# Optimization experiments

Hardware: AMD Instinct MI355X
Metric: run time of the kernel (lower is better)

## Reference

```python
import jax, jax.numpy as jnp
import numpy as np

DILATIONS = (1, 2, 4, 8, 16, 32, 64, 128, 256)
R = 128          # residual/skip channels
K = 3            # kernel size
B, CIN, T = 8, 1, 16384
COUT = 1
L = len(DILATIONS)


def causal_conv(x, w, b, dilation):
    # x: [B, Cin, T], w: [Cout, Cin, K] -> [B, Cout, T], left-padded (causal)
    k = w.shape[-1]
    pad = dilation * (k - 1)
    y = jax.lax.conv_general_dilated(
        x, w, window_strides=(1,), padding=[(pad, 0)],
        rhs_dilation=(dilation,), dimension_numbers=("NCH", "OIH", "NCH"))
    return y + b[None, :, None]


def setup_inputs() -> dict:
    key = jax.random.key(0)
    ks = jax.random.split(key, 11)
    s = 0.1  # weight scale to keep gated activations in a healthy range
    return {
        "x": jax.random.normal(ks[0], (B, CIN, T), jnp.float32),
        "input_w": s * jax.random.normal(ks[1], (R, CIN, 1), jnp.float32),
        "input_b": s * jax.random.normal(ks[2], (R,), jnp.float32),
        "conv_w": s * jax.random.normal(ks[3], (L, 2 * R, R, K), jnp.float32),
        "conv_b": s * jax.random.normal(ks[4], (L, 2 * R), jnp.float32),
        "out_w": s * jax.random.normal(ks[5], (L, R, R, 1), jnp.float32),
        "out_b": s * jax.random.normal(ks[6], (L, R), jnp.float32),
        "output1_w": s * jax.random.normal(ks[7], (R, R * L, 1), jnp.float32),
        "output1_b": s * jax.random.normal(ks[8], (R,), jnp.float32),
        "output2_w": s * jax.random.normal(ks[9], (COUT, R, 1), jnp.float32),
        "output2_b": s * jax.random.normal(ks[10], (COUT,), jnp.float32),
    }


def reference(x, input_w, input_b, conv_w, conv_b, out_w, out_b,
              output1_w, output1_b, output2_w, output2_b):
    # input layer: 1x1 conv + tanh (use_output_transform=False)
    h = jnp.tanh(causal_conv(x, input_w, input_b, 1))

    skips = []
    for i, d in enumerate(DILATIONS):
        pre = causal_conv(h, conv_w[i], conv_b[i], d)      # [B, 2R, T]
        t, g = jnp.split(pre, 2, axis=1)
        z = jnp.tanh(t) * jax.nn.sigmoid(g)                # gated activation
        skips.append(z)                                     # skip = activation out
        res = causal_conv(z, out_w[i], out_b[i], 1)         # 1x1 output transform
        h = h + res                                         # residual connection

    sk = jnp.concatenate(skips, axis=1)                     # [B, R*L, T]
    y = jnp.tanh(causal_conv(sk, output1_w, output1_b, 1))
    out = causal_conv(y, output2_w, output2_b, 1)           # linear
    return out
```

## Files before the change

### kernel.cpp

```cpp
#include <hip/hip_runtime.h>
#include <cstdint>
#include <cstddef>

#define T_LEN 16384
#define BATCH 8
#define NLAYER 9

typedef _Float16 f16;
typedef __attribute__((ext_vector_type(8))) _Float16 f16x8;
typedef __attribute__((ext_vector_type(4))) float f32x4;
#define MFMA_F16 __builtin_amdgcn_mfma_f32_16x16x32_f16

__device__ __forceinline__ float fast_sigmoid(float x) {
    return 1.0f / (1.0f + __expf(-x));
}
__device__ __forceinline__ float fast_tanh(float x) {
    return 1.0f - 2.0f / (__expf(2.0f * x) + 1.0f);
}

__device__ __forceinline__ void stage16(const f16* g, f16* l) {
    __builtin_amdgcn_global_load_lds(
        (const __attribute__((address_space(1))) unsigned int*)g,
        (__attribute__((address_space(3))) unsigned int*)l, 16, 0, 0);
}

__global__ __launch_bounds__(256) void prep_weights(
    const float* __restrict__ cw, const float* __restrict__ ow,
    const float* __restrict__ o1w, f16* __restrict__ wA, f16* __restrict__ wB)
{
    int n = blockIdx.x * 256 + threadIdx.x;
    const int NA = NLAYER * 12 * 256 * 32;
    const int NB = NLAYER * 4 * 256 * 32;
    if (n < NA) {
        int kp = n & 31; int q = n >> 5;
        int c = q & 255; q >>= 8;
        int ch = q % 12; int l = q / 12;
        int i = kp >> 3, j = kp & 7;
        int il = i ^ ((c >> 1) & 3);
        int kpl = il * 8 + j;
        int tap = ch >> 2;
        int r = (ch & 3) * 32 + kpl;
        wA[n] = (f16)cw[((size_t)(l * 256 + c) * 128 + r) * 3 + tap];
    } else if (n < NA + NB) {
        int m = n - NA;
        int kp = m & 31; int q = m >> 5;
        int c = q & 255; q >>= 8;
        int ch = q & 3; int l = q >> 2;
        int k = ch * 32 + kp;
        float v = (c < 128) ? ow[(size_t)(l * 128 + c) * 128 + k]
                            : o1w[(size_t)(c - 128) * 1152 + l * 128 + k];
        wB[m] = (f16)v;
    }
}

__global__ __launch_bounds__(256) void input_init(
    const float* __restrict__ x, const float* __restrict__ iw,
    const float* __restrict__ ib,
    f16* __restrict__ h, f16* __restrict__ acc1)
{
    int n = blockIdx.x * 256 + threadIdx.x;
    int r = n & 127; int bt = n >> 7;
    h[n] = (f16)fast_tanh(iw[r] * x[bt] + ib[r]);
    acc1[n] = (f16)0.0f;
}

__global__ __launch_bounds__(256, 4) void layer_kernel(
    const f16* __restrict__ h_in, f16* __restrict__ h_out,
    f16* __restrict__ acc1,
    const f16* __restrict__ wA,
    const f16* __restrict__ wB,
    const float* __restrict__ cb,
    const float* __restrict__ ob,
    int d)
{
    __shared__ __align__(16) char smem_raw[32768];
    f16* const Bsm = (f16*)smem_raw;
    f16* const zs  = (f16*)smem_raw;

    const int tid  = threadIdx.x;
    const int lane = tid & 63;
    const int w4   = tid >> 6;
    const int mg   = w4 & 1;
    const int ng   = w4 >> 1;
    const int col  = lane & 15;
    const int quad = lane >> 4;
    const int b    = blockIdx.y;
    const int bx   = blockIdx.x;
    const int xt   = ((bx & 7) << 5) | (bx >> 3);
    const int t0   = xt * 64;

    const f16* hb = h_in + (size_t)b * T_LEN * 128;

    const int bswz = (quad ^ ((col >> 1) & 3)) * 8;

    f32x4 acc[2][8];
#pragma unroll
    for (int mt = 0; mt < 2; ++mt)
#pragma unroll
        for (int nt = 0; nt < 8; ++nt) acc[mt][nt] = (f32x4)0.0f;

    {
        const f16* src = wA + w4 * 2048 + lane * 8;
        f16* dst = Bsm + w4 * 2048;
#pragma unroll
        for (int i = 0; i < 4; ++i) stage16(src + i * 512, dst + i * 512);
    }

#pragma unroll
    for (int tap = 0; tap < 3; ++tap) {
        const int off = (2 - tap) * d;
        f16x8 a[2][4];
#pragma unroll
        for (int c = 0; c < 4; ++c) {
            const int ch = tap * 4 + c;
            __builtin_amdgcn_sched_barrier(0);
            asm volatile("s_waitcnt vmcnt(0)" ::: "memory");
            __builtin_amdgcn_s_barrier();
            __builtin_amdgcn_sched_barrier(0);
            if (ch < 11) {
                const f16* src = wA + (ch + 1) * 8192 + w4 * 2048 + lane * 8;
                f16* dst = Bsm + ((ch + 1) & 1) * 8192 + w4 * 2048;
#pragma unroll
                for (int i = 0; i < 4; ++i) stage16(src + i * 512, dst + i * 512);
            }
            if (c == 0) {
#pragma unroll
                for (int mt = 0; mt < 2; ++mt) {
                    int t = t0 + mg * 32 + mt * 16 + col - off;
                    if (t >= 0) {
                        const f16* hp = &hb[(size_t)t * 128 + quad * 8];
#pragma unroll
                        for (int cc = 0; cc < 4; ++cc)
                            a[mt][cc] = *(const f16x8*)&hp[cc * 32];
                    } else {
#pragma unroll
                        for (int cc = 0; cc < 4; ++cc)
                            a[mt][cc] = (f16x8)(f16)0.0f;
                    }
                }
            }
            const f16* bsc = Bsm + (ch & 1) * 8192;
#pragma unroll
            for (int nt = 0; nt < 8; ++nt) {
                int nb = (nt < 4) ? (ng * 64 + nt * 16)
                                  : (128 + ng * 64 + (nt - 4) * 16);
                f16x8 bf = *(const f16x8*)&bsc[(nb + col) * 32 + bswz];
                acc[0][nt] = MFMA_F16(a[0][c], bf, acc[0][nt], 0, 0, 0);
                acc[1][nt] = MFMA_F16(a[1][c], bf, acc[1][nt], 0, 0, 0);
            }
        }
    }
    __syncthreads();

#pragma unroll
    for (int nt = 0; nt < 4; ++nt) {
        int j = ng * 64 + nt * 16 + col;
        float cf = cb[j];
        float cg = cb[j + 128];
#pragma unroll
        for (int mt = 0; mt < 2; ++mt)
#pragma unroll
            for (int reg = 0; reg < 4; ++reg) {
                float f = acc[mt][nt][reg]     + cf;
                float g = acc[mt][nt + 4][reg] + cg;
                zs[(mg * 32 + mt * 16 + quad * 4 + reg) * 136 + j] =
                    (f16)(fast_tanh(f) * fast_sigmoid(g));
            }
    }
    __syncthreads();

#pragma unroll
    for (int mt = 0; mt < 2; ++mt)
#pragma unroll
        for (int nt = 0; nt < 8; ++nt) acc[mt][nt] = (f32x4)0.0f;

#pragma unroll
    for (int ch = 0; ch < 4; ++ch) {
        f16x8 a[2];
#pragma unroll
        for (int mt = 0; mt < 2; ++mt)
            a[mt] = *(const f16x8*)&zs[(mg * 32 + mt * 16 + col) * 136 + ch * 32 + quad * 8];
        const f16* wc = wB + ch * 8192;
#pragma unroll
        for (int nt = 0; nt < 8; ++nt) {
            int nb = (nt < 4) ? (ng * 64 + nt * 16)
                              : (128 + ng * 64 + (nt - 4) * 16);
            f16x8 bf = *(const f16x8*)&wc[(nb + col) * 32 + quad * 8];
            acc[0][nt] = MFMA_F16(a[0], bf, acc[0][nt], 0, 0, 0);
            acc[1][nt] = MFMA_F16(a[1], bf, acc[1][nt], 0, 0, 0);
        }
    }
    __syncthreads();

#pragma unroll
    for (int nt = 0; nt < 4; ++nt) {
        int n = ng * 64 + nt * 16 + col;
        float o = ob[n];
#pragma unroll
        for (int mt = 0; mt < 2; ++mt)
#pragma unroll
            for (int reg = 0; reg < 4; ++reg)
                zs[(mg * 32 + mt * 16 + quad * 4 + reg) * 136 + n] =
                    (f16)(acc[mt][nt][reg] + o);
    }
    __syncthreads();
    const int orow = tid >> 2, oseg = tid & 3;
    const size_t gb = (size_t)b * T_LEN * 128 + (size_t)(t0 + orow) * 128 + oseg * 32;
#pragma unroll
    for (int i = 0; i < 4; ++i) {
        f16x8 rv = *(const f16x8*)&zs[orow * 136 + oseg * 32 + i * 8];
        f16x8 hv = *(const f16x8*)&h_in[gb + i * 8];
        *(f16x8*)&h_out[gb + i * 8] = hv + rv;
    }
    __syncthreads();

#pragma unroll
    for (int nt = 0; nt < 4; ++nt) {
        int n = ng * 64 + nt * 16 + col;
#pragma unroll
        for (int mt = 0; mt < 2; ++mt)
#pragma unroll
            for (int reg = 0; reg < 4; ++reg)
                zs[(mg * 32 + mt * 16 + quad * 4 + reg) * 136 + n] =
                    (f16)acc[mt][nt + 4][reg];
    }
    __syncthreads();
#pragma unroll
    for (int i = 0; i < 4; ++i) {
        f16x8 sv2 = *(const f16x8*)&zs[orow * 136 + oseg * 32 + i * 8];
        f16x8 av  = *(const f16x8*)&acc1[gb + i * 8];
        *(f16x8*)&acc1[gb + i * 8] = av + sv2;
    }
}

__global__ __launch_bounds__(256) void final_kernel(
    const f16* __restrict__ acc1, const float* __restrict__ b1,
    const float* __restrict__ w2, const float* __restrict__ b2,
    float* __restrict__ out)
{
    int lane = threadIdx.x & 63;
    int w = threadIdx.x >> 6;
    int bt = blockIdx.x * 4 + w;
    float v0 = (float)acc1[(size_t)bt * 128 + lane];
    float v1 = (float)acc1[(size_t)bt * 128 + lane + 64];
    float s = w2[lane] * fast_tanh(v0 + b1[lane]) +
              w2[lane + 64] * fast_tanh(v1 + b1[lane + 64]);
#pragma unroll
    for (int k = 1; k < 64; k <<= 1) s += __shfl_xor(s, k, 64);
    if (lane == 0) out[bt] = s + b2[0];
}

extern "C" void kernel_launch(void* const* d_in, const int* in_sizes, int n_in,
                              void* d_out, int out_size, void* d_ws, size_t ws_size,
                              hipStream_t stream)
{
    const float* x   = (const float*)d_in[0];
    const float* iw  = (const float*)d_in[1];
    const float* ib  = (const float*)d_in[2];
    const float* cw  = (const float*)d_in[3];
    const float* cb  = (const float*)d_in[4];
    const float* ow  = (const float*)d_in[5];
    const float* ob  = (const float*)d_in[6];
    const float* o1w = (const float*)d_in[7];
    const float* o1b = (const float*)d_in[8];
    const float* o2w = (const float*)d_in[9];
    const float* o2b = (const float*)d_in[10];
    float* out = (float*)d_out;

    const size_t HTR = (size_t)BATCH * T_LEN * 128;
    f16* hA   = (f16*)d_ws;
    f16* hB   = hA + HTR;
    f16* acc1 = hB + HTR;
    f16* wAp  = acc1 + HTR;
    f16* wBp  = wAp + (size_t)NLAYER * 12 * 256 * 32;

    prep_weights<<<4608, 256, 0, stream>>>(cw, ow, o1w, wAp, wBp);
    input_init<<<65536, 256, 0, stream>>>(x, iw, ib, hA, acc1);

    const int DIL[NLAYER] = {1, 2, 4, 8, 16, 32, 64, 128, 256};
    f16* hin = hA; f16* hout = hB;
    for (int l = 0; l < NLAYER; ++l) {
        layer_kernel<<<dim3(T_LEN / 64, BATCH), 256, 0, stream>>>(
            hin, hout, acc1,
            wAp + (size_t)l * 12 * 256 * 32, wBp + (size_t)l * 4 * 256 * 32,
            cb + l * 256, ob + l * 128, DIL[l]);
        f16* tmp = hin; hin = hout; hout = tmp;
    }
    final_kernel<<<BATCH * T_LEN / 4, 256, 0, stream>>>(acc1, o1b, o2w, o2b, out);
}
```

Before: 812.7 us.

## Deepen weight staging pipeline, prefetch taps, merge epilogue LDS passes

```diff
diff --git a/kernel.cpp b/kernel.cpp
--- a/kernel.cpp
+++ b/kernel.cpp
@@ -11,17 +11,14 @@
 typedef __attribute__((ext_vector_type(4))) float f32x4;
 #define MFMA_F16 __builtin_amdgcn_mfma_f32_16x16x32_f16
 
-__device__ __forceinline__ float fast_sigmoid(float x) {
-    return 1.0f / (1.0f + __expf(-x));
-}
-__device__ __forceinline__ float fast_tanh(float x) {
-    return 1.0f - 2.0f / (__expf(2.0f * x) + 1.0f);
-}
-
 __device__ __forceinline__ void stage16(const f16* g, f16* l) {
     __builtin_amdgcn_global_load_lds(
         (const __attribute__((address_space(1))) unsigned int*)g,
         (__attribute__((address_space(3))) unsigned int*)l, 16, 0, 0);
+}
+
+__device__ __forceinline__ float fast_tanh(float x) {
+    return 1.0f - 2.0f / (__expf(2.0f * x) + 1.0f);
 }
 
 __global__ __launch_bounds__(256) void prep_weights(
@@ -73,9 +70,10 @@
     const float* __restrict__ ob,
     int d)
 {
-    __shared__ __align__(16) char smem_raw[32768];
+    __shared__ __align__(16) char smem_raw[34816];
     f16* const Bsm = (f16*)smem_raw;
-    f16* const zs  = (f16*)smem_raw;
+    f16* const zsR = (f16*)smem_raw;
+    f16* const zsS = (f16*)smem_raw + 8704;
 
     const int tid  = threadIdx.x;
     const int lane = tid & 63;
@@ -90,7 +88,6 @@
     const int t0   = xt * 64;
 
     const f16* hb = h_in + (size_t)b * T_LEN * 128;
-
     const int bswz = (quad ^ ((col >> 1) & 3)) * 8;
 
     f32x4 acc[2][8];
@@ -99,56 +96,64 @@
 #pragma unroll
         for (int nt = 0; nt < 8; ++nt) acc[mt][nt] = (f32x4)0.0f;
 
+    f16x8 a[2][4];
+    auto loadA = [&](int tap) {
+        const int off = (2 - tap) * d;
+#pragma unroll
+        for (int mt = 0; mt < 2; ++mt) {
+            int t = t0 + mg * 32 + mt * 16 + col - off;
+            int tc = t < 0 ? 0 : t;
+            const f16* hp = &hb[(size_t)tc * 128 + quad * 8];
+#pragma unroll
+            for (int cc = 0; cc < 4; ++cc) {
+                f16x8 v = *(const f16x8*)&hp[cc * 32];
+                a[mt][cc] = (t >= 0) ? v : (f16x8)(f16)0.0f;
+            }
+        }
+    };
+
     {
-        const f16* src = wA + w4 * 2048 + lane * 8;
-        f16* dst = Bsm + w4 * 2048;
-#pragma unroll
-        for (int i = 0; i < 4; ++i) stage16(src + i * 512, dst + i * 512);
-    }
-
-#pragma unroll
-    for (int tap = 0; tap < 3; ++tap) {
-        const int off = (2 - tap) * d;
-        f16x8 a[2][4];
-#pragma unroll
-        for (int c = 0; c < 4; ++c) {
-            const int ch = tap * 4 + c;
-            __builtin_amdgcn_sched_barrier(0);
+        const f16* s0 = wA + w4 * 1024 + lane * 8;
+        f16* d0 = Bsm + w4 * 1024;
+        stage16(s0, d0); stage16(s0 + 512, d0 + 512);
+        const f16* s1 = wA + 4096 + w4 * 1024 + lane * 8;
+        f16* d1 = Bsm + 4096 + w4 * 1024;
+        stage16(s1, d1); stage16(s1 + 512, d1 + 512);
+        __builtin_amdgcn_sched_barrier(0);
+        loadA(0);
+        __builtin_amdgcn_sched_barrier(0);
+        asm volatile("s_waitcnt vmcnt(10)" ::: "memory");
+        __builtin_amdgcn_s_barrier();
+        __builtin_amdgcn_sched_barrier(0);
+    }
+
+#pragma unroll
+    for (int hc = 0; hc < 24; ++hc) {
+        if (hc == 8) loadA(1);
+        if (hc == 16) loadA(2);
+        if (hc + 2 < 24) {
+            const f16* s = wA + (hc + 2) * 4096 + w4 * 1024 + lane * 8;
+            f16* dd = Bsm + ((hc + 2) & 3) * 4096 + w4 * 1024;
+            stage16(s, dd); stage16(s + 512, dd + 512);
+        }
+        const f16* bsc = Bsm + (hc & 3) * 4096;
+        const int c = (hc >> 1) & 3;
+        const int nbase = (hc & 1) * 4;
+#pragma unroll
+        for (int ntl = 0; ntl < 4; ++ntl) {
+            int row = ng * 64 + ntl * 16 + col;
+            f16x8 bf = *(const f16x8*)&bsc[row * 32 + bswz];
+            acc[0][nbase + ntl] = MFMA_F16(a[0][c], bf, acc[0][nbase + ntl], 0, 0, 0);
+            acc[1][nbase + ntl] = MFMA_F16(a[1][c], bf, acc[1][nbase + ntl], 0, 0, 0);
+        }
+        __builtin_amdgcn_sched_barrier(0);
+        if (hc == 22) {
             asm volatile("s_waitcnt vmcnt(0)" ::: "memory");
-            __builtin_amdgcn_s_barrier();
-            __builtin_amdgcn_sched_barrier(0);
-            if (ch < 11) {
-                const f16* src = wA + (ch + 1) * 8192 + w4 * 2048 + lane * 8;
-                f16* dst = Bsm + ((ch + 1) & 1) * 8192 + w4 * 2048;
-#pragma unroll
-                for (int i = 0; i < 4; ++i) stage16(src + i * 512, dst + i * 512);
-            }
-            if (c == 0) {
-#pragma unroll
-                for (int mt = 0; mt < 2; ++mt) {
-                    int t = t0 + mg * 32 + mt * 16 + col - off;
-                    if (t >= 0) {
-                        const f16* hp = &hb[(size_t)t * 128 + quad * 8];
-#pragma unroll
-                        for (int cc = 0; cc < 4; ++cc)
-                            a[mt][cc] = *(const f16x8*)&hp[cc * 32];
-                    } else {
-#pragma unroll
-                        for (int cc = 0; cc < 4; ++cc)
-                            a[mt][cc] = (f16x8)(f16)0.0f;
-                    }
-                }
-            }
-            const f16* bsc = Bsm + (ch & 1) * 8192;
-#pragma unroll
-            for (int nt = 0; nt < 8; ++nt) {
-                int nb = (nt < 4) ? (ng * 64 + nt * 16)
-                                  : (128 + ng * 64 + (nt - 4) * 16);
-                f16x8 bf = *(const f16x8*)&bsc[(nb + col) * 32 + bswz];
-                acc[0][nt] = MFMA_F16(a[0][c], bf, acc[0][nt], 0, 0, 0);
-                acc[1][nt] = MFMA_F16(a[1][c], bf, acc[1][nt], 0, 0, 0);
-            }
-        }
+        } else if (hc < 22) {
+            asm volatile("s_waitcnt vmcnt(2)" ::: "memory");
+        }
+        if (hc < 23) __builtin_amdgcn_s_barrier();
+        __builtin_amdgcn_sched_barrier(0);
     }
     __syncthreads();
 
@@ -163,8 +168,11 @@
             for (int reg = 0; reg < 4; ++reg) {
                 float f = acc[mt][nt][reg]     + cf;
                 float g = acc[mt][nt + 4][reg] + cg;
-                zs[(mg * 32 + mt * 16 + quad * 4 + reg) * 136 + j] =
-                    (f16)(fast_tanh(f) * fast_sigmoid(g));
+                float E = __builtin_amdgcn_exp2f(2.885390082f * f);
+                float S = __builtin_amdgcn_exp2f(1.442695041f * g);
+                float z = (E - 1.0f) * S *
+                          __builtin_amdgcn_rcpf((E + 1.0f) * (S + 1.0f));
+                zsR[(mg * 32 + mt * 16 + quad * 4 + reg) * 136 + j] = (f16)z;
             }
     }
     __syncthreads();
@@ -176,18 +184,18 @@
 
 #pragma unroll
     for (int ch = 0; ch < 4; ++ch) {
-        f16x8 a[2];
+        f16x8 a2[2];
 #pragma unroll
         for (int mt = 0; mt < 2; ++mt)
-            a[mt] = *(const f16x8*)&zs[(mg * 32 + mt * 16 + col) * 136 + ch * 32 + quad * 8];
+            a2[mt] = *(const f16x8*)&zsR[(mg * 32 + mt * 16 + col) * 136 + ch * 32 + quad * 8];
         const f16* wc = wB + ch * 8192;
 #pragma unroll
         for (int nt = 0; nt < 8; ++nt) {
             int nb = (nt < 4) ? (ng * 64 + nt * 16)
                               : (128 + ng * 64 + (nt - 4) * 16);
             f16x8 bf = *(const f16x8*)&wc[(nb + col) * 32 + quad * 8];
-            acc[0][nt] = MFMA_F16(a[0], bf, acc[0][nt], 0, 0, 0);
-            acc[1][nt] = MFMA_F16(a[1], bf, acc[1][nt], 0, 0, 0);
+            acc[0][nt] = MFMA_F16(a2[0], bf, acc[0][nt], 0, 0, 0);
+            acc[1][nt] = MFMA_F16(a2[1], bf, acc[1][nt], 0, 0, 0);
         }
     }
     __syncthreads();
@@ -199,37 +207,29 @@
 #pragma unroll
         for (int mt = 0; mt < 2; ++mt)
 #pragma unroll
-            for (int reg = 0; reg < 4; ++reg)
-                zs[(mg * 32 + mt * 16 + quad * 4 + reg) * 136 + n] =
-                    (f16)(acc[mt][nt][reg] + o);
+            for (int reg = 0; reg < 4; ++reg) {
+                int r = (mg * 32 + mt * 16 + quad * 4 + reg) * 136 + n;
+                zsR[r] = (f16)(acc[mt][nt][reg] + o);
+                zsS[r] = (f16)acc[mt][nt + 4][reg];
+            }
     }
     __syncthreads();
     const int orow = tid >> 2, oseg = tid & 3;
     const size_t gb = (size_t)b * T_LEN * 128 + (size_t)(t0 + orow) * 128 + oseg * 32;
+    f16x8 hv[4], av[4];
+#pragma unroll
+    for (int i = 0; i < 4; ++i) hv[i] = *(const f16x8*)&h_in[gb + i * 8];
+#pragma unroll
+    for (int i = 0; i < 4; ++i) av[i] = *(const f16x8*)&acc1[gb + i * 8];
 #pragma unroll
     for (int i = 0; i < 4; ++i) {
-        f16x8 rv = *(const f16x8*)&zs[orow * 136 + oseg * 32 + i * 8];
-        f16x8 hv = *(const f16x8*)&h_in[gb + i * 8];
-        *(f16x8*)&h_out[gb + i * 8] = hv + rv;
-    }
-    __syncthreads();
-
-#pragma unroll
-    for (int nt = 0; nt < 4; ++nt) {
-        int n = ng * 64 + nt * 16 + col;
-#pragma unroll
-        for (int mt = 0; mt < 2; ++mt)
-#pragma unroll
-            for (int reg = 0; reg < 4; ++reg)
-                zs[(mg * 32 + mt * 16 + quad * 4 + reg) * 136 + n] =
-                    (f16)acc[mt][nt + 4][reg];
-    }
-    __syncthreads();
+        f16x8 rv = *(const f16x8*)&zsR[orow * 136 + oseg * 32 + i * 8];
+        *(f16x8*)&h_out[gb + i * 8] = hv[i] + rv;
+    }
 #pragma unroll
     for (int i = 0; i < 4; ++i) {
-        f16x8 sv2 = *(const f16x8*)&zs[orow * 136 + oseg * 32 + i * 8];
-        f16x8 av  = *(const f16x8*)&acc1[gb + i * 8];
-        *(f16x8*)&acc1[gb + i * 8] = av + sv2;
+        f16x8 sv = *(const f16x8*)&zsS[orow * 136 + oseg * 32 + i * 8];
+        *(f16x8*)&acc1[gb + i * 8] = av[i] + sv;
     }
 }
 
```

Measured after the change: 754.8 us. -7.1%, faster.
